# Kernel optimization log

Hardware: AMD Instinct MI355X
Metric: run time of the kernel (lower is better)

The kernel has to match this reference:

```python
import jax, jax.numpy as jnp
import numpy as np

B, N, C = 4, 16384, 512
HEADS = 16
HEADC = C // HEADS
HIDDEN = int(C * 4.0)


def setup_inputs() -> dict:
    key = jax.random.key(0)
    ks = jax.random.split(key, 8)
    s1 = 1.0 / np.sqrt(C)
    s2 = 1.0 / np.sqrt(HIDDEN)
    return {
        "x": jax.random.normal(ks[0], (B, N, C), jnp.float32),
        "mask_matrix": jnp.zeros((1,), jnp.int32),
        "norm1_w": jnp.ones((C,), jnp.float32),
        "norm1_b": jnp.zeros((C,), jnp.float32),
        "kln_w": jnp.ones((HEADS, 1, HEADC), jnp.float32),
        "kln_b": jnp.zeros((HEADS, 1, HEADC), jnp.float32),
        "vln_w": jnp.ones((HEADS, 1, HEADC), jnp.float32),
        "vln_b": jnp.zeros((HEADS, 1, HEADC), jnp.float32),
        "norm2_w": jnp.ones((C,), jnp.float32),
        "norm2_b": jnp.zeros((C,), jnp.float32),
        "fc1_w": jax.random.uniform(ks[1], (HIDDEN, C), jnp.float32, -s1, s1),
        "fc1_b": jax.random.uniform(ks[2], (HIDDEN,), jnp.float32, -s1, s1),
        "fc2_w": jax.random.uniform(ks[3], (C, HIDDEN), jnp.float32, -s2, s2),
        "fc2_b": jax.random.uniform(ks[4], (C,), jnp.float32, -s2, s2),
    }


def _ln(t, w, b, eps=1e-5):
    # standard nn.LayerNorm: biased variance, eps inside sqrt
    mean = t.mean(-1, keepdims=True)
    var = ((t - mean) ** 2).mean(-1, keepdims=True)
    return w * (t - mean) / jnp.sqrt(var + eps) + b


def _ln_std(t, w, b, eps=1e-5):
    # custom LayerNorm: unbiased std (torch.std), eps added to std
    d = t.shape[-1]
    mean = t.mean(-1, keepdims=True)
    var = ((t - mean) ** 2).sum(-1, keepdims=True) / (d - 1)
    return w * ((t - mean) / (jnp.sqrt(var) + eps)) + b


def reference(x, mask_matrix, norm1_w, norm1_b, kln_w, kln_b, vln_w, vln_b,
              norm2_w, norm2_b, fc1_w, fc1_b, fc2_w, fc2_b):
    b, n, c = x.shape
    shortcut = x
    h = _ln(x, norm1_w, norm1_b)
    # simple_attn (softmax-free linear attention)
    qkv = h.reshape(b, n, HEADS, HEADC).transpose(0, 2, 1, 3)  # [B,H,N,D]
    q = qkv
    k = _ln_std(qkv, kln_w, kln_b)
    v = _ln_std(qkv, vln_w, vln_b)
    kv = jnp.einsum('bhnd,bhne->bhde', k, v) / n        # [B,H,D,D]
    attn = jnp.einsum('bhnd,bhde->bhne', q, kv)          # [B,H,N,D]
    attn = attn.transpose(0, 2, 1, 3).reshape(b, n, c)
    h = attn + h                                          # residual inside simple_attn (bias = x post-norm1)
    x = shortcut + h
    # MLP branch
    m = _ln(x, norm2_w, norm2_b)
    m = jax.nn.gelu(m @ fc1_w.T + fc1_b, approximate=False)
    m = m @ fc2_w.T + fc2_b
    return x + m
```

## Files before the change

kernel.cpp:

```cpp
#include <hip/hip_runtime.h>
#include <cstdint>

#define BB 4
#define NN 16384
#define CC 512
#define HH 16
#define DD 32
#define HID 2048
#define MTOT (BB * NN)
#define MCHUNK 16384

typedef __bf16 bf16_t;
typedef __bf16 bf16x8 __attribute__((ext_vector_type(8)));
typedef __bf16 bf16x4 __attribute__((ext_vector_type(4)));
typedef float  f32x4  __attribute__((ext_vector_type(4)));

__device__ __forceinline__ void gload_lds16(const void* g, void* l) {
  auto gp = reinterpret_cast<const __attribute__((address_space(1))) char*>(
      reinterpret_cast<uintptr_t>(g));
  auto lp = reinterpret_cast<__attribute__((address_space(3))) char*>(
      reinterpret_cast<uintptr_t>(l));
  __builtin_amdgcn_global_load_lds(gp, lp, 16, 0, 0);
}

__global__ __launch_bounds__(256) void cvt_bf16_kernel(const float* __restrict__ src,
                                                       bf16_t* __restrict__ dst) {
  const long i = ((long)blockIdx.x * 256 + threadIdx.x) * 4;
  const f32x4 v = *(const f32x4*)(src + i);
  bf16x4 o;
  o[0] = (bf16_t)v[0]; o[1] = (bf16_t)v[1]; o[2] = (bf16_t)v[2]; o[3] = (bf16_t)v[3];
  *(bf16x4*)(dst + i) = o;
}

__global__ __launch_bounds__(256) void norm1_kernel(const float* __restrict__ x,
                                                    const float* __restrict__ w,
                                                    const float* __restrict__ bvec,
                                                    bf16_t* __restrict__ h) {
  const int wv = threadIdx.x >> 6, l = threadIdx.x & 63;
  const long tok = (long)blockIdx.x * 4 + wv;
  const int c0 = l * 8;
  const f32x4 a = *(const f32x4*)(x + tok * CC + c0);
  const f32x4 b = *(const f32x4*)(x + tok * CC + c0 + 4);
  float v[8];
#pragma unroll
  for (int i = 0; i < 4; ++i) { v[i] = a[i]; v[4 + i] = b[i]; }
  float s = 0.f, s2 = 0.f;
#pragma unroll
  for (int i = 0; i < 8; ++i) { s += v[i]; s2 += v[i] * v[i]; }
  for (int off = 32; off; off >>= 1) { s += __shfl_xor(s, off); s2 += __shfl_xor(s2, off); }
  const float mean = s * (1.f / CC);
  const float var  = fmaxf(s2 * (1.f / CC) - mean * mean, 0.f);
  const float rstd = rsqrtf(var + 1e-5f);
  const f32x4 w0 = *(const f32x4*)(w + c0), w1 = *(const f32x4*)(w + c0 + 4);
  const f32x4 b0 = *(const f32x4*)(bvec + c0), b1 = *(const f32x4*)(bvec + c0 + 4);
  bf16x8 o;
#pragma unroll
  for (int i = 0; i < 4; ++i) {
    o[i]     = (bf16_t)(w0[i] * (v[i] - mean) * rstd + b0[i]);
    o[4 + i] = (bf16_t)(w1[i] * (v[4 + i] - mean) * rstd + b1[i]);
  }
  *(bf16x8*)(h + tok * CC + c0) = o;
}

__global__ __launch_bounds__(256) void kv_partial_kernel(const bf16_t* __restrict__ h,
                                                         const float* __restrict__ klw,
                                                         const float* __restrict__ klb,
                                                         const float* __restrict__ vlw,
                                                         const float* __restrict__ vlb,
                                                         float* __restrict__ kvp) {
  __shared__ bf16_t kb[256 * 32];
  __shared__ bf16_t vb[256 * 32];
  __shared__ float scratch[192 * 16];
  const int tid = threadIdx.x;
  const int bh = blockIdx.x >> 6, chunk = blockIdx.x & 63;
  const int head = bh & 15;
  const int b = bh >> 4;
  const long tok0 = ((long)b << 14) + chunk * 256;
  const bf16_t* src = h + (tok0 + tid) * (long)CC + head * DD;
  float hv[32];
  {
    float s = 0.f, s2 = 0.f;
#pragma unroll
    for (int c = 0; c < 4; ++c) {
      const bf16x8 r = *(const bf16x8*)(src + c * 8);
#pragma unroll
      for (int j = 0; j < 8; ++j) {
        hv[c * 8 + j] = (float)r[j]; s += hv[c * 8 + j]; s2 += hv[c * 8 + j] * hv[c * 8 + j];
      }
    }
    const float mean = s * (1.f / 32.f);
    const float varu = fmaxf((s2 - 32.f * mean * mean) * (1.f / 31.f), 0.f);
    const float inv = 1.f / (sqrtf(varu) + 1e-5f);
    const int sx = (tid >> 1) & 3;
#pragma unroll
    for (int c = 0; c < 4; ++c) {
      bf16x8 kc, vc;
#pragma unroll
      for (int j = 0; j < 8; ++j) {
        const int d = c * 8 + j;
        const float t = (hv[d] - mean) * inv;
        kc[j] = (bf16_t)(klw[head * DD + d] * t + klb[head * DD + d]);
        vc[j] = (bf16_t)(vlw[head * DD + d] * t + vlb[head * DD + d]);
      }
      *(bf16x8*)((char*)kb + tid * 64 + ((c ^ sx) * 16)) = kc;
      *(bf16x8*)((char*)vb + tid * 64 + ((c ^ sx) * 16)) = vc;
    }
  }
  __syncthreads();
  const int g = tid >> 6, l = tid & 63;
  const int d0 = (l >> 3) * 4, e0 = (l & 7) * 4;
  const int ck = (l >> 3) >> 1, hk = (l >> 3) & 1;
  const int ce = (l & 7) >> 1, he = l & 1;
  float a[4][4] = {};
  for (int t = g; t < 256; t += 4) {
    const int tx = (t >> 1) & 3;
    const bf16x4 kq = *(const bf16x4*)((const char*)kb + t * 64 + ((ck ^ tx) * 16) + hk * 8);
    const bf16x4 vq = *(const bf16x4*)((const char*)vb + t * 64 + ((ce ^ tx) * 16) + he * 8);
    float kf[4], vf[4];
#pragma unroll
    for (int i2 = 0; i2 < 4; ++i2) { kf[i2] = (float)kq[i2]; vf[i2] = (float)vq[i2]; }
#pragma unroll
    for (int i2 = 0; i2 < 4; ++i2)
#pragma unroll
      for (int j2 = 0; j2 < 4; ++j2) a[i2][j2] += kf[i2] * vf[j2];
  }
  __syncthreads();
  if (g) {
#pragma unroll
    for (int i2 = 0; i2 < 4; ++i2)
#pragma unroll
      for (int j2 = 0; j2 < 4; ++j2)
        scratch[((g - 1) * 64 + l) * 16 + i2 * 4 + j2] = a[i2][j2];
  }
  __syncthreads();
  if (!g) {
#pragma unroll
    for (int gg = 0; gg < 3; ++gg)
#pragma unroll
      for (int i2 = 0; i2 < 4; ++i2)
#pragma unroll
        for (int j2 = 0; j2 < 4; ++j2)
          a[i2][j2] += scratch[(gg * 64 + l) * 16 + i2 * 4 + j2];
    float* dst = kvp + ((long)(bh * 64 + chunk) << 10);
#pragma unroll
    for (int i2 = 0; i2 < 4; ++i2) {
      f32x4 st;
      st[0] = a[i2][0]; st[1] = a[i2][1]; st[2] = a[i2][2]; st[3] = a[i2][3];
      *(f32x4*)&dst[(d0 + i2) * 32 + e0] = st;
    }
  }
}

__global__ __launch_bounds__(256) void kv_reduce_kernel(const float* __restrict__ kvp,
                                                        bf16_t* __restrict__ kvT) {
  const int bh = blockIdx.x;
  const int i4 = threadIdx.x * 4;
  const int d = i4 >> 5, e0 = i4 & 31;
  float s[4] = {};
  const float* p = kvp + ((long)bh << 16) + i4;
  for (int ch = 0; ch < 64; ++ch) {
    const f32x4 t = *(const f32x4*)(p + (ch << 10));
    s[0] += t[0]; s[1] += t[1]; s[2] += t[2]; s[3] += t[3];
  }
  const float sc = 1.f / (float)NN;
  bf16_t* q = kvT + ((long)bh << 10);
#pragma unroll
  for (int j = 0; j < 4; ++j) q[(e0 + j) * 32 + d] = (bf16_t)(s[j] * sc);
}

#define ASTRIDE 520
__global__ __launch_bounds__(256) void attn_fused_kernel(const float* __restrict__ x,
                                                         const bf16_t* __restrict__ h,
                                                         const bf16_t* __restrict__ kvTg,
                                                         const float* __restrict__ n2w,
                                                         const float* __restrict__ n2b,
                                                         float* __restrict__ xout,
                                                         bf16_t* __restrict__ mout) {
  __shared__ bf16_t attn_s[32 * ASTRIDE];
  const int tid = threadIdx.x;
  const int wv = tid >> 6, lane = tid & 63;
  const int lr = lane & 15, kg = lane >> 4;
  const long tok0 = (long)blockIdx.x * 32;
  const int b = (int)(tok0 >> 14);
  const bf16_t* kvsrc = kvTg + ((long)b << 14);

  {
    const int tt = wv & 1, hh = wv >> 1;
    const bf16_t* arow = h + (tok0 + tt * 16 + lr) * (long)CC + kg * 8;
    const f32x4 zero = {};
#pragma unroll
    for (int hi = 0; hi < 8; ++hi) {
      const int hd = hh * 8 + hi;
      const bf16_t* kvh = kvsrc + (hd << 10) + kg * 8;
      const bf16x8 af = *(const bf16x8*)(arow + hd * DD);
      const bf16x8 b0 = *(const bf16x8*)(kvh + lr * 32);
      const bf16x8 b1 = *(const bf16x8*)(kvh + (16 + lr) * 32);
      const f32x4 a0 = __builtin_amdgcn_mfma_f32_16x16x32_bf16(af, b0, zero, 0, 0, 0);
      const f32x4 a1 = __builtin_amdgcn_mfma_f32_16x16x32_bf16(af, b1, zero, 0, 0, 0);
      const int rbase = tt * 16 + kg * 4;
#pragma unroll
      for (int rg = 0; rg < 4; ++rg) {
        attn_s[(rbase + rg) * ASTRIDE + hd * 32 + lr]      = (bf16_t)a0[rg];
        attn_s[(rbase + rg) * ASTRIDE + hd * 32 + 16 + lr] = (bf16_t)a1[rg];
      }
    }
  }
  __syncthreads();

  const int c0 = lane * 8;
  const f32x4 w0 = *(const f32x4*)(n2w + c0), w1 = *(const f32x4*)(n2w + c0 + 4);
  const f32x4 bb0 = *(const f32x4*)(n2b + c0), bb1 = *(const f32x4*)(n2b + c0 + 4);
  for (int it = 0; it < 8; ++it) {
    const int tl = wv * 8 + it;
    const long tok = tok0 + tl;
    const f32x4 xa = *(const f32x4*)(x + tok * CC + c0);
    const f32x4 xb = *(const f32x4*)(x + tok * CC + c0 + 4);
    const bf16x8 hv = *(const bf16x8*)(h + tok * CC + c0);
    const bf16x8 av = *(const bf16x8*)&attn_s[tl * ASTRIDE + c0];
    float x2[8];
#pragma unroll
    for (int i = 0; i < 4; ++i) {
      x2[i]     = xa[i] + (float)hv[i]     + (float)av[i];
      x2[4 + i] = xb[i] + (float)hv[4 + i] + (float)av[4 + i];
    }
    float s = 0.f, s2 = 0.f;
#pragma unroll
    for (int i = 0; i < 8; ++i) { s += x2[i]; s2 += x2[i] * x2[i]; }
    for (int off = 32; off; off >>= 1) { s += __shfl_xor(s, off); s2 += __shfl_xor(s2, off); }
    const float mean = s * (1.f / CC);
    const float var  = fmaxf(s2 * (1.f / CC) - mean * mean, 0.f);
    const float rstd = rsqrtf(var + 1e-5f);
    f32x4 oa, ob;
    bf16x8 om;
#pragma unroll
    for (int i = 0; i < 4; ++i) {
      oa[i] = x2[i]; ob[i] = x2[4 + i];
      om[i]     = (bf16_t)(w0[i] * (x2[i] - mean) * rstd + bb0[i]);
      om[4 + i] = (bf16_t)(w1[i] * (x2[4 + i] - mean) * rstd + bb1[i]);
    }
    *(f32x4*)(xout + tok * CC + c0) = oa;
    *(f32x4*)(xout + tok * CC + c0 + 4) = ob;
    *(bf16x8*)(mout + tok * CC + c0) = om;
  }
}

template <int K, int NOUT, int BN, bool GELU>
__global__ __launch_bounds__(512, 2) void gemm8p_kernel(const bf16_t* __restrict__ A,
                                                        const bf16_t* __restrict__ Bw,
                                                        const float* __restrict__ bias,
                                                        bf16_t* __restrict__ outb,
                                                        float* __restrict__ outf) {
  constexpr int NTILE = NOUT / BN;
  constexpr int NT = K / 64;
  constexpr int NI = NT / 2;
  constexpr int WNSPAN = BN / 4;
  constexpr int NH = WNSPAN / 32;
  constexpr int NREP = 2 * NH;
  constexpr int BLOADS = BN / 128;
  constexpr int ABYT = 32768;
  constexpr int BBYT = BN * 128;
  constexpr int BUFB = ABYT + BBYT;
  constexpr int WVM = 2 + BLOADS;

  __shared__ char lds[2 * BUFB];

  const int tid = threadIdx.x;
  const int wid = tid >> 6, lane = tid & 63;
  const int wm = wid >> 2, wn = wid & 3;
  const int lr = lane & 15, kg = lane >> 4;

  int bid = blockIdx.x;
  const int qq = gridDim.x >> 3;
  bid = (bid & 7) * qq + (bid >> 3);
  const long row0 = (long)(bid / NTILE) * 256;
  const long col0 = (long)(bid % NTILE) * BN;

  const int srow = tid >> 2;
  const int sce = (((tid & 3) ^ ((srow >> 1) & 3)) << 3);
  const bf16_t* pA = A + (row0 + srow) * (long)K + sce;
  const bf16_t* pB = Bw + (col0 + srow) * (long)K + sce;
  char* ldsp = (char*)lds;

  auto SA = [&](int buf, int ks, int kt) {
    char* d_ = ldsp + buf * BUFB + ks * 16384 + tid * 16;
    const bf16_t* g_ = pA + (long)kt * 64 + ks * 32;
    gload_lds16(g_, d_);
    gload_lds16(g_ + 128L * K, d_ + 8192);
  };
  auto SB = [&](int buf, int ks, int kt) {
    char* d_ = ldsp + buf * BUFB + ABYT + ks * (BN * 64) + tid * 16;
    const bf16_t* g_ = pB + (long)kt * 64 + ks * 32;
    gload_lds16(g_, d_);
    if constexpr (BLOADS == 2) gload_lds16(g_ + 128L * K, d_ + 8192);
  };

  f32x4 acc[8][NREP] = {};
  bf16x8 af[8], bf[NH];

  auto LDA8 = [&](int buf, int ks) {
    const char* b_ = ldsp + buf * BUFB + ks * 16384;
#pragma unroll
    for (int m = 0; m < 8; ++m) {
      const int row = wm * 128 + m * 16 + lr;
      af[m] = *(const bf16x8*)(b_ + row * 64 + ((kg ^ ((row >> 1) & 3)) << 4));
    }
  };
  auto LDBN = [&](int buf, int ks, int nh) {
    const char* b_ = ldsp + buf * BUFB + ABYT + ks * (BN * 64);
#pragma unroll
    for (int n = 0; n < NH; ++n) {
      const int row = wn * WNSPAN + nh * (WNSPAN / 2) + n * 16 + lr;
      bf[n] = *(const bf16x8*)(b_ + row * 64 + ((kg ^ ((row >> 1) & 3)) << 4));
    }
  };
  auto MM = [&](int nh) {
    __builtin_amdgcn_s_setprio(1);
#pragma unroll
    for (int m = 0; m < 8; ++m)
#pragma unroll
      for (int n = 0; n < NH; ++n)
        acc[m][nh * NH + n] =
            __builtin_amdgcn_mfma_f32_16x16x32_bf16(af[m], bf[n], acc[m][nh * NH + n], 0, 0, 0);
    __builtin_amdgcn_s_setprio(0);
  };
  auto WVMW = [&]() {
    if constexpr (WVM == 4) asm volatile("s_waitcnt vmcnt(4)" ::: "memory");
    else                    asm volatile("s_waitcnt vmcnt(3)" ::: "memory");
  };
#define BARX() __builtin_amdgcn_s_barrier()
#define LGKM0() asm volatile("s_waitcnt lgkmcnt(0)" ::: "memory")

  SA(0, 0, 0); SA(0, 1, 0); SB(0, 0, 0); SB(0, 1, 0);
  SA(1, 0, 1); SB(1, 0, 1);
  WVMW();
  BARX();

  for (int i = 0; i < NI; ++i) {
    const int t1 = 2 * i + 1, tA = 2 * i + 2, tB = 2 * i + 3;
    const bool last = (i == NI - 1);
    LDA8(0, 0); LDBN(0, 0, 0); SA(1, 1, t1);
    BARX(); LGKM0(); MM(0); BARX();
    LDBN(0, 0, 1); SB(1, 1, t1);
    BARX(); LGKM0(); MM(1); BARX();
    LDA8(0, 1); LDBN(0, 1, 0); if (tA < NT) SA(0, 0, tA);
    BARX(); LGKM0(); MM(0); BARX();
    LDBN(0, 1, 1); if (tA < NT) SB(0, 0, tA);
    BARX(); LGKM0(); MM(1);
    if (last) asm volatile("s_waitcnt vmcnt(0)" ::: "memory"); else WVMW();
    BARX();
    LDA8(1, 0); LDBN(1, 0, 0); if (tA < NT) SA(0, 1, tA);
    BARX(); LGKM0(); MM(0); BARX();
    LDBN(1, 0, 1); if (tA < NT) SB(0, 1, tA);
    BARX(); LGKM0(); MM(1); BARX();
    LDA8(1, 1); LDBN(1, 1, 0); if (tB < NT) SA(1, 0, tB);
    BARX(); LGKM0(); MM(0); BARX();
    LDBN(1, 1, 1); if (tB < NT) SB(1, 0, tB);
    BARX(); LGKM0(); MM(1);
    if (!last) { WVMW(); BARX(); }
  }
#undef BARX
#undef LGKM0

#pragma unroll
  for (int j = 0; j < NREP; ++j) {
    const long col = col0 + wn * WNSPAN + j * 16 + lr;
    const float bs = bias[col];
#pragma unroll
    for (int m = 0; m < 8; ++m) {
#pragma unroll
      for (int rg = 0; rg < 4; ++rg) {
        const long row = row0 + wm * 128 + m * 16 + kg * 4 + rg;
        const float v = acc[m][j][rg] + bs;
        if constexpr (GELU) {
          const float u = 0.7978845608028654f * (v + 0.044715f * v * v * v);
          const float gv = v / (1.f + __expf(-2.f * u));
          outb[row * NOUT + col] = (bf16_t)gv;
        } else {
          outf[row * NOUT + col] += v;
        }
      }
    }
  }
}

extern "C" void kernel_launch(void* const* d_in, const int* in_sizes, int n_in,
                              void* d_out, int out_size, void* d_ws, size_t ws_size,
                              hipStream_t stream) {
  const float* x   = (const float*)d_in[0];
  const float* n1w = (const float*)d_in[2];
  const float* n1b = (const float*)d_in[3];
  const float* klw = (const float*)d_in[4];
  const float* klb = (const float*)d_in[5];
  const float* vlw = (const float*)d_in[6];
  const float* vlb = (const float*)d_in[7];
  const float* n2w = (const float*)d_in[8];
  const float* n2b = (const float*)d_in[9];
  const float* w1f = (const float*)d_in[10];
  const float* b1  = (const float*)d_in[11];
  const float* w2f = (const float*)d_in[12];
  const float* b2  = (const float*)d_in[13];
  float* out = (float*)d_out;

  char* ws = (char*)d_ws;
  bf16_t* h   = (bf16_t*)(ws);
  bf16_t* mb  = (bf16_t*)(ws + (size_t)67108864);
  bf16_t* act = (bf16_t*)(ws + (size_t)134217728);
  bf16_t* w1  = (bf16_t*)(ws + (size_t)201326592);
  bf16_t* w2  = (bf16_t*)(ws + (size_t)203423744);
  float*  kvp = (float*)(ws + (size_t)205520896);
  bf16_t* kvT = (bf16_t*)(ws + (size_t)222298112);

  cvt_bf16_kernel<<<1024, 256, 0, stream>>>(w1f, w1);
  cvt_bf16_kernel<<<1024, 256, 0, stream>>>(w2f, w2);
  norm1_kernel<<<MTOT / 4, 256, 0, stream>>>(x, n1w, n1b, h);
  kv_partial_kernel<<<BB * HH * 64, 256, 0, stream>>>(h, klw, klb, vlw, vlb, kvp);
  kv_reduce_kernel<<<BB * HH, 256, 0, stream>>>(kvp, kvT);
  attn_fused_kernel<<<MTOT / 32, 256, 0, stream>>>(x, h, kvT, n2w, n2b, out, mb);
  for (int ch = 0; ch < MTOT / MCHUNK; ++ch) {
    gemm8p_kernel<CC, HID, 256, true>
        <<<(MCHUNK / 256) * (HID / 256), 512, 0, stream>>>(
        mb + (long)ch * MCHUNK * CC, w1, b1, act, nullptr);
    gemm8p_kernel<HID, CC, 128, false>
        <<<(MCHUNK / 256) * (CC / 128), 512, 0, stream>>>(
        act, w2, b2, nullptr, out + (long)ch * MCHUNK * CC);
  }
}
```

Measured before the change: 638.9 us.

## Deepen GEMM prefetch waits and size MLP chunks from workspace size

The GEMM main loop now waits on vmcnt after every half-tile stage with deeper outstanding-load allowances (8/6 instead of 4/3). This keeps more global-to-LDS loads in flight and overlaps them with MFMA work. On the host side, the M-chunk count for the MLP GEMMs is chosen from the available workspace (1, 2 or 4 chunks), and the second GEMM uses BN=256 when chunks are large. Fewer, larger launches cut launch and tail overhead, at the cost of a larger activation buffer and more reliance on the vmcnt accounting being exact.

New measurement: 600.6 us. 6.0% less time.

```diff
diff --git a/kernel.cpp b/kernel.cpp
--- a/kernel.cpp
+++ b/kernel.cpp
@@ -8,7 +8,6 @@
 #define DD 32
 #define HID 2048
 #define MTOT (BB * NN)
-#define MCHUNK 16384
 
 typedef __bf16 bf16_t;
 typedef __bf16 bf16x8 __attribute__((ext_vector_type(8)));
@@ -260,7 +259,6 @@
   constexpr int ABYT = 32768;
   constexpr int BBYT = BN * 128;
   constexpr int BUFB = ABYT + BBYT;
-  constexpr int WVM = 2 + BLOADS;
 
   __shared__ char lds[2 * BUFB];
 
@@ -323,43 +321,52 @@
             __builtin_amdgcn_mfma_f32_16x16x32_bf16(af[m], bf[n], acc[m][nh * NH + n], 0, 0, 0);
     __builtin_amdgcn_s_setprio(0);
   };
-  auto WVMW = [&]() {
-    if constexpr (WVM == 4) asm volatile("s_waitcnt vmcnt(4)" ::: "memory");
-    else                    asm volatile("s_waitcnt vmcnt(3)" ::: "memory");
+  auto W2U = [&]() {
+    if constexpr (BLOADS == 2) asm volatile("s_waitcnt vmcnt(8)" ::: "memory");
+    else                       asm volatile("s_waitcnt vmcnt(6)" ::: "memory");
+  };
+  auto W1U = [&]() {
+    if constexpr (BLOADS == 2) asm volatile("s_waitcnt vmcnt(4)" ::: "memory");
+    else                       asm volatile("s_waitcnt vmcnt(3)" ::: "memory");
   };
 #define BARX() __builtin_amdgcn_s_barrier()
 #define LGKM0() asm volatile("s_waitcnt lgkmcnt(0)" ::: "memory")
-
-  SA(0, 0, 0); SA(0, 1, 0); SB(0, 0, 0); SB(0, 1, 0);
+#define W0U() asm volatile("s_waitcnt vmcnt(0)" ::: "memory")
+
+  SA(0, 0, 0); SB(0, 0, 0);
+  SA(0, 1, 0); SB(0, 1, 0);
   SA(1, 0, 1); SB(1, 0, 1);
-  WVMW();
+  W2U();
   BARX();
 
   for (int i = 0; i < NI; ++i) {
     const int t1 = 2 * i + 1, tA = 2 * i + 2, tB = 2 * i + 3;
-    const bool last = (i == NI - 1);
     LDA8(0, 0); LDBN(0, 0, 0); SA(1, 1, t1);
     BARX(); LGKM0(); MM(0); BARX();
     LDBN(0, 0, 1); SB(1, 1, t1);
-    BARX(); LGKM0(); MM(1); BARX();
+    BARX(); LGKM0(); MM(1); W2U(); BARX();
     LDA8(0, 1); LDBN(0, 1, 0); if (tA < NT) SA(0, 0, tA);
     BARX(); LGKM0(); MM(0); BARX();
     LDBN(0, 1, 1); if (tA < NT) SB(0, 0, tA);
     BARX(); LGKM0(); MM(1);
-    if (last) asm volatile("s_waitcnt vmcnt(0)" ::: "memory"); else WVMW();
+    if (tA < NT) W2U(); else W1U();
     BARX();
     LDA8(1, 0); LDBN(1, 0, 0); if (tA < NT) SA(0, 1, tA);
     BARX(); LGKM0(); MM(0); BARX();
     LDBN(1, 0, 1); if (tA < NT) SB(0, 1, tA);
-    BARX(); LGKM0(); MM(1); BARX();
+    BARX(); LGKM0(); MM(1);
+    if (tA < NT) W2U(); else W0U();
+    BARX();
     LDA8(1, 1); LDBN(1, 1, 0); if (tB < NT) SA(1, 0, tB);
     BARX(); LGKM0(); MM(0); BARX();
     LDBN(1, 1, 1); if (tB < NT) SB(1, 0, tB);
     BARX(); LGKM0(); MM(1);
-    if (!last) { WVMW(); BARX(); }
+    if (tB < NT) W2U();
+    BARX();
   }
 #undef BARX
 #undef LGKM0
+#undef W0U
 
 #pragma unroll
   for (int j = 0; j < NREP; ++j) {
@@ -401,14 +408,21 @@
   const float* b2  = (const float*)d_in[13];
   float* out = (float*)d_out;
 
+  int nch;
+  if (ws_size >= 423755776ULL)      nch = 1;
+  else if (ws_size >= 289538048ULL) nch = 2;
+  else                              nch = 4;
+  const long mch = MTOT / nch;
+
   char* ws = (char*)d_ws;
-  bf16_t* h   = (bf16_t*)(ws);
-  bf16_t* mb  = (bf16_t*)(ws + (size_t)67108864);
-  bf16_t* act = (bf16_t*)(ws + (size_t)134217728);
-  bf16_t* w1  = (bf16_t*)(ws + (size_t)201326592);
-  bf16_t* w2  = (bf16_t*)(ws + (size_t)203423744);
-  float*  kvp = (float*)(ws + (size_t)205520896);
-  bf16_t* kvT = (bf16_t*)(ws + (size_t)222298112);
+  size_t off = 0;
+  bf16_t* h   = (bf16_t*)(ws + off); off += (size_t)MTOT * CC * 2;
+  bf16_t* mb  = (bf16_t*)(ws + off); off += (size_t)MTOT * CC * 2;
+  bf16_t* act = (bf16_t*)(ws + off); off += (size_t)mch * HID * 2;
+  bf16_t* w1  = (bf16_t*)(ws + off); off += (size_t)HID * CC * 2;
+  bf16_t* w2  = (bf16_t*)(ws + off); off += (size_t)HID * CC * 2;
+  float*  kvp = (float*)(ws + off);  off += (size_t)BB * HH * 64 * 1024 * 4;
+  bf16_t* kvT = (bf16_t*)(ws + off);
 
   cvt_bf16_kernel<<<1024, 256, 0, stream>>>(w1f, w1);
   cvt_bf16_kernel<<<1024, 256, 0, stream>>>(w2f, w2);
@@ -416,12 +430,18 @@
   kv_partial_kernel<<<BB * HH * 64, 256, 0, stream>>>(h, klw, klb, vlw, vlb, kvp);
   kv_reduce_kernel<<<BB * HH, 256, 0, stream>>>(kvp, kvT);
   attn_fused_kernel<<<MTOT / 32, 256, 0, stream>>>(x, h, kvT, n2w, n2b, out, mb);
-  for (int ch = 0; ch < MTOT / MCHUNK; ++ch) {
+  for (int ch = 0; ch < nch; ++ch) {
     gemm8p_kernel<CC, HID, 256, true>
-        <<<(MCHUNK / 256) * (HID / 256), 512, 0, stream>>>(
-        mb + (long)ch * MCHUNK * CC, w1, b1, act, nullptr);
-    gemm8p_kernel<HID, CC, 128, false>
-        <<<(MCHUNK / 256) * (CC / 128), 512, 0, stream>>>(
-        act, w2, b2, nullptr, out + (long)ch * MCHUNK * CC);
-  }
-}
+        <<<(int)((mch / 256) * (HID / 256)), 512, 0, stream>>>(
+        mb + (size_t)ch * mch * CC, w1, b1, act, nullptr);
+    if (mch >= 32768) {
+      gemm8p_kernel<HID, CC, 256, false>
+          <<<(int)((mch / 256) * (CC / 256)), 512, 0, stream>>>(
+          act, w2, b2, nullptr, out + (size_t)ch * mch * CC);
+    } else {
+      gemm8p_kernel<HID, CC, 128, false>
+          <<<(int)((mch / 256) * (CC / 128)), 512, 0, stream>>>(
+          act, w2, b2, nullptr, out + (size_t)ch * mch * CC);
+    }
+  }
+}
```
